# Optimization experiments

Hardware: AMD Instinct MI355X
Metric: run time of the kernel (lower is better)

## Reference

```python
import jax, jax.numpy as jnp
import numpy as np

B = 4096          # graphs (frames)
NPG = 22          # players per frame
N = B * NPG       # total nodes
E = B * NPG * (NPG - 1)
D_BB = 256        # backbone_dout == GRNN hidden
D_NODE = 128      # raw node feature dim
D_PROJ = 256      # cfg.proj_dout
D_GIN = 64        # glob_din
D_GOUT = 128      # cfg.glob_dout
D_IN = D_BB + D_PROJ  # GRNN input dim = 512


def setup_inputs() -> dict:
    key = jax.random.key(0)
    ks = jax.random.split(key, 24)
    def w(k, shape):
        return jax.random.normal(k, shape, jnp.float32) * 0.05
    inp = {
        "z": jax.random.normal(ks[0], (N, D_BB), jnp.float32),
        "u": jax.random.normal(ks[1], (B, D_GIN), jnp.float32),
        "x": jax.random.normal(ks[2], (N, D_NODE), jnp.float32),
        # edge_index is unused math-wise because GConvGRU is built with K=1 ChebConvs
        "edge_index": jax.random.randint(ks[3], (2, E), 0, N, dtype=jnp.int32),
        "batch": jnp.repeat(jnp.arange(B, dtype=jnp.int32), NPG),
        "batch_size": B,
        "prev_h": jax.random.normal(ks[4], (N, D_BB), jnp.float32),
        # fusion params
        "w_proj": w(ks[5], (D_NODE, D_PROJ)), "b_proj": jnp.zeros((D_PROJ,), jnp.float32),
        "w_glob": w(ks[6], (D_GIN, D_GOUT)), "b_glob": jnp.zeros((D_GOUT,), jnp.float32),
        # GConvGRU (K=1 ChebConv == linear) gate params: update z, reset r, candidate h
        "W_xz": w(ks[7], (D_IN, D_BB)),  "b_xz": jnp.zeros((D_BB,), jnp.float32),
        "W_hz": w(ks[8], (D_BB, D_BB)),  "b_hz": jnp.zeros((D_BB,), jnp.float32),
        "W_xr": w(ks[9], (D_IN, D_BB)),  "b_xr": jnp.zeros((D_BB,), jnp.float32),
        "W_hr": w(ks[10], (D_BB, D_BB)), "b_hr": jnp.zeros((D_BB,), jnp.float32),
        "W_xh": w(ks[11], (D_IN, D_BB)), "b_xh": jnp.zeros((D_BB,), jnp.float32),
        "W_hh": w(ks[12], (D_BB, D_BB)), "b_hh": jnp.zeros((D_BB,), jnp.float32),
    }
    return inp


def reference(z, u, x, edge_index, batch, batch_size, prev_h,
              w_proj, b_proj, w_glob, b_glob,
              W_xz, b_xz, W_hz, b_hz,
              W_xr, b_xr, W_hr, b_hr,
              W_xh, b_xh, W_hh, b_hh):
    # --- GraphGlobalFusion: mean readout + relu(Linear(u)) + concat ---
    sums = jax.ops.segment_sum(z, batch, num_segments=batch_size)            # [B, D_BB]
    cnts = jax.ops.segment_sum(jnp.ones((z.shape[0], 1), z.dtype), batch,
                               num_segments=batch_size)                      # [B, 1]
    graph_emb = sums / jnp.maximum(cnts, 1.0)
    glob_emb = jax.nn.relu(u @ w_glob + b_glob)                              # [B, D_GOUT]
    fused = jnp.concatenate([graph_emb, glob_emb], axis=-1)                  # [B, D_BB+D_GOUT]

    # --- node mode: raw feature projection, then GConvGRU (K=1 -> linear gates) ---
    x_proj = jax.nn.relu(x @ w_proj + b_proj)                                # [N, D_PROJ]
    xin = jnp.concatenate([z, x_proj], axis=-1)                              # [N, D_IN]
    Z = jax.nn.sigmoid(xin @ W_xz + b_xz + prev_h @ W_hz + b_hz)
    R = jax.nn.sigmoid(xin @ W_xr + b_xr + prev_h @ W_hr + b_hr)
    H_tilde = jnp.tanh(xin @ W_xh + b_xh + (prev_h * R) @ W_hh + b_hh)
    h = Z * prev_h + (1.0 - Z) * H_tilde                                     # [N, D_BB]
    return (fused, h)
```

## Files before the change

### kernel.cpp

```cpp
#include <hip/hip_runtime.h>
#include <hip/hip_bf16.h>

#define NNODES 90112
#define BGRAPH 4096
#define NPG 22
#define DBB 256
#define DNODE 128
#define DPROJ 256
#define DGIN 64
#define DGOUT 128

#define WTG_OFF   32768
#define WTHH_OFF  622592
#define WS_BF16_ELEMS 688128

typedef __attribute__((ext_vector_type(8))) short bf16x8;
typedef __attribute__((ext_vector_type(4))) short bf16x4;
typedef __attribute__((ext_vector_type(4))) float f32x4;
typedef __attribute__((ext_vector_type(2))) float f32x2;

__device__ __forceinline__ short f2bf(float f) {
  __hip_bfloat16 h = __float2bfloat16(f);
  return *reinterpret_cast<short*>(&h);
}
__device__ __forceinline__ float bf2f(short s) {
  union { unsigned int u; float f; } c;
  c.u = ((unsigned int)(unsigned short)s) << 16;
  return c.f;
}
__device__ __forceinline__ float fsig(float xv) {
  return __fdividef(1.0f, 1.0f + __expf(-xv));
}
__device__ __forceinline__ float ftanh(float xv) {
  return 1.0f - __fdividef(2.0f, __expf(2.0f * xv) + 1.0f);
}

#define DMA16(gsrc, ldst)                                                        \
  __builtin_amdgcn_global_load_lds(                                              \
      (const __attribute__((address_space(1))) void*)(gsrc),                     \
      (__attribute__((address_space(3))) void*)(ldst), 16, 0, 0)

template<int N>
__device__ __forceinline__ void vmwaitN() {
  static_assert(N >= 0 && N <= 6, "vmcnt range");
  if constexpr (N == 0) asm volatile("s_waitcnt vmcnt(0)" ::: "memory");
  else if constexpr (N == 1) asm volatile("s_waitcnt vmcnt(1)" ::: "memory");
  else if constexpr (N == 2) asm volatile("s_waitcnt vmcnt(2)" ::: "memory");
  else if constexpr (N == 3) asm volatile("s_waitcnt vmcnt(3)" ::: "memory");
  else if constexpr (N == 4) asm volatile("s_waitcnt vmcnt(4)" ::: "memory");
  else if constexpr (N == 5) asm volatile("s_waitcnt vmcnt(5)" ::: "memory");
  else asm volatile("s_waitcnt vmcnt(6)" ::: "memory");
  __builtin_amdgcn_sched_barrier(0);
}
#define LBAR() do { asm volatile("s_waitcnt lgkmcnt(0)" ::: "memory");           \
                    __builtin_amdgcn_s_barrier(); } while (0)

__global__ void pack_weights(const float* __restrict__ w_proj,
                             const float* __restrict__ W_xz, const float* __restrict__ W_hz,
                             const float* __restrict__ W_xr, const float* __restrict__ W_hr,
                             const float* __restrict__ W_xh, const float* __restrict__ W_hh,
                             const float* __restrict__ b_xz, const float* __restrict__ b_hz,
                             const float* __restrict__ b_xr, const float* __restrict__ b_hr,
                             const float* __restrict__ b_xh, const float* __restrict__ b_hh,
                             __hip_bfloat16* __restrict__ wsb, float* __restrict__ wsf) {
  int i = blockIdx.x * 256 + threadIdx.x;
  if (i < 32768) {
    int c = i >> 7, k = i & 127;
    wsb[i] = __float2bfloat16(w_proj[k * DPROJ + c]);
  } else if (i < WTHH_OFF) {
    int j = i - WTG_OFF;
    int kc  = j / 24576;
    int rem = j - kc * 24576;
    int ct  = rem >> 9;
    int q   = rem & 511;
    int l   = q >> 3, e = q & 7;
    int l15 = l & 15, kg = l >> 4;
    int k   = kc * 32 + kg * 8 + e;
    int g   = ct >> 4;
    int c   = (ct & 15) * 16 + l15;
    float v;
    if (g == 0)      v = (k < 512) ? W_xz[k * 256 + c] : W_hz[(k - 512) * 256 + c];
    else if (g == 1) v = (k < 512) ? W_xr[k * 256 + c] : W_hr[(k - 512) * 256 + c];
    else             v = (k < 512) ? W_xh[k * 256 + c] : 0.0f;
    wsb[i] = __float2bfloat16(v);
  } else if (i < WS_BF16_ELEMS) {
    int j = i - WTHH_OFF;
    int kc  = j >> 13;
    int rem = j & 8191;
    int ct  = rem >> 9;
    int q   = rem & 511;
    int l   = q >> 3, e = q & 7;
    int l15 = l & 15, kg = l >> 4;
    int k   = kc * 32 + kg * 8 + e;
    int c   = ct * 16 + l15;
    wsb[i] = __float2bfloat16(W_hh[k * 256 + c]);
  }
  if (i < 256) {
    wsf[i]       = b_xz[i] + b_hz[i];
    wsf[256 + i] = b_xr[i] + b_hr[i];
    wsf[512 + i] = b_xh[i] + b_hh[i];
  }
}

__global__ void fused_head(const float* __restrict__ z, const float* __restrict__ u,
                           const float* __restrict__ w_glob, const float* __restrict__ b_glob,
                           float* __restrict__ out) {
  int b = blockIdx.x;
  int t = threadIdx.x;
  __shared__ float us[DGIN];
  if (t < DGIN) us[t] = u[b * DGIN + t];
  __syncthreads();
  const float* zb = z + (size_t)b * NPG * DBB;
  #pragma unroll
  for (int half = 0; half < 2; ++half) {
    int c = t + half * 128;
    float s = 0.f;
    #pragma unroll
    for (int r = 0; r < NPG; ++r) s += zb[r * DBB + c];
    out[(size_t)b * 384 + c] = s * (1.0f / NPG);
  }
  float acc = b_glob[t];
  #pragma unroll
  for (int k = 0; k < DGIN; ++k) acc += us[k] * w_glob[k * DGOUT + t];
  out[(size_t)b * 384 + 256 + t] = fmaxf(acc, 0.f);
}

#define MFMA16(a, b, c) __builtin_amdgcn_mfma_f32_16x16x32_bf16(a, b, c, 0, 0, 0)

template<int KC>
__device__ __forceinline__ void gstep(
    const float* __restrict__ z, const float* __restrict__ prev_h,
    const __hip_bfloat16* __restrict__ wpk,
    __hip_bfloat16* Wb, __hip_bfloat16* ActC, __hip_bfloat16* XP,
    int tid, int r0, int l15, int lg, int wid, int lane,
    f32x4 (&accz)[4], f32x4 (&accr)[4], f32x4 (&acch)[4]) {
  constexpr int  KN       = KC + 1;
  constexpr bool do_stage = (KN >= 1 && KN <= 7) || (KN >= 16 && KN <= 23);
  constexpr bool bar      = (KC >= 1 && KC <= 7) || (KC >= 15 && KC <= 23);
  constexpr bool staged   = (KC < 8) || (KC >= 16);
  constexpr bool has_h    = (KC < 16);
  constexpr int NZ = (KC <= 14) ? 5 : (KC == 15) ? 4 : (KC <= 22) ? 3 : 1;
  constexpr int NR = (KC <= 14) ? 5 : (KC == 15) ? 4 : (KC <= 21) ? 3 : (KC == 22) ? 2 : 0;
  constexpr int NH = (KC <= 14) ? 5 : 4;

  f32x2 sl;
  int srow = tid >> 4, sc2 = (tid & 15) * 2;
  if constexpr (do_stage) {
    const float* src = (KN < 8) ? z : prev_h;
    constexpr int kofs = (KN < 8 ? KN : KN - 16) * 32;
    sl = *(const f32x2*)(src + (size_t)(r0 + srow) * DBB + kofs + sc2);
  }
  if constexpr (bar) LBAR();

  bf16x8 act[4];
  #pragma unroll
  for (int rt = 0; rt < 4; ++rt) {
    const int row = rt * 16 + l15;
    if constexpr (staged)
      act[rt] = *(const bf16x8*)&ActC[(KC % 3) * (64 * 40) + row * 40 + lg * 8];
    else {
      const int gk = (KC - 8) * 4 + lg;
      act[rt] = *(const bf16x8*)&XP[row * 256 + ((gk ^ (row & 7)) * 8)];
    }
  }

  vmwaitN<NZ>();
  {
    bf16x8 w = *(const bf16x8*)&Wb[((KC & 1) * 3 + 0) * 8192 + wid * 512 + lane * 8];
    __builtin_amdgcn_s_setprio(1);
    #pragma unroll
    for (int rt = 0; rt < 4; ++rt) accz[rt] = MFMA16(w, act[rt], accz[rt]);
    __builtin_amdgcn_s_setprio(0);
  }
  if constexpr (KC + 2 <= 23)
    DMA16(wpk + (((size_t)(KC + 2) * 48 + 0 * 16 + wid) * 64 + lane) * 8,
          Wb + (((KC + 2) & 1) * 3 + 0) * 8192 + wid * 512);

  vmwaitN<NR>();
  {
    bf16x8 w = *(const bf16x8*)&Wb[((KC & 1) * 3 + 1) * 8192 + wid * 512 + lane * 8];
    __builtin_amdgcn_s_setprio(1);
    #pragma unroll
    for (int rt = 0; rt < 4; ++rt) accr[rt] = MFMA16(w, act[rt], accr[rt]);
    __builtin_amdgcn_s_setprio(0);
  }
  if constexpr (KC + 2 <= 23)
    DMA16(wpk + (((size_t)(KC + 2) * 48 + 1 * 16 + wid) * 64 + lane) * 8,
          Wb + (((KC + 2) & 1) * 3 + 1) * 8192 + wid * 512);

  if constexpr (has_h) {
    vmwaitN<NH>();
    bf16x8 w = *(const bf16x8*)&Wb[((KC & 1) * 3 + 2) * 8192 + wid * 512 + lane * 8];
    __builtin_amdgcn_s_setprio(1);
    #pragma unroll
    for (int rt = 0; rt < 4; ++rt) acch[rt] = MFMA16(w, act[rt], acch[rt]);
    __builtin_amdgcn_s_setprio(0);
    if constexpr (KC + 2 <= 15)
      DMA16(wpk + (((size_t)(KC + 2) * 48 + 2 * 16 + wid) * 64 + lane) * 8,
            Wb + (((KC + 2) & 1) * 3 + 2) * 8192 + wid * 512);
  }

  if constexpr (do_stage) {
    unsigned int pk = (unsigned int)(unsigned short)f2bf(sl[0]) |
                      ((unsigned int)(unsigned short)f2bf(sl[1]) << 16);
    *(unsigned int*)&ActC[(KN % 3) * (64 * 40) + srow * 40 + sc2] = pk;
  }
}

template<int S>
__device__ __forceinline__ void hstep(
    const __hip_bfloat16* __restrict__ hpk, __hip_bfloat16* Wb, __hip_bfloat16* XP,
    int l15, int lg, int wid, int lane, f32x4 (&acch)[4]) {
  constexpr int NW = (S <= 5) ? 2 : (S == 6) ? 1 : 0;
  bf16x8 act[4];
  #pragma unroll
  for (int rt = 0; rt < 4; ++rt) {
    const int row = rt * 16 + l15;
    const int gk = S * 4 + lg;
    act[rt] = *(const bf16x8*)&XP[row * 256 + ((gk ^ (row & 7)) * 8)];
  }
  vmwaitN<NW>();
  bf16x8 w = *(const bf16x8*)&Wb[(S % 4) * 8192 + wid * 512 + lane * 8];
  __builtin_amdgcn_s_setprio(1);
  #pragma unroll
  for (int rt = 0; rt < 4; ++rt) acch[rt] = MFMA16(w, act[rt], acch[rt]);
  __builtin_amdgcn_s_setprio(0);
  if constexpr (S + 3 <= 7)
    DMA16(hpk + (((size_t)(S + 3) * 16 + wid) * 64 + lane) * 8,
          Wb + ((S + 3) % 4) * 8192 + wid * 512);
}

__global__ __launch_bounds__(1024)
void grnn_main(const float* __restrict__ z, const float* __restrict__ x,
               const float* __restrict__ prev_h, const float* __restrict__ b_proj,
               const __hip_bfloat16* __restrict__ wsb, const float* __restrict__ wsf,
               float* __restrict__ h_out) {
  __shared__ __align__(16) __hip_bfloat16 Wb[6 * 8192];
  __shared__ __align__(16) __hip_bfloat16 Xs[64 * 128];
  __shared__ __align__(16) __hip_bfloat16 XP[64 * 256];
  __shared__ __align__(16) __hip_bfloat16 ActC[3 * 64 * 40];

  const int r0   = blockIdx.x * 64;
  const int tid  = threadIdx.x;
  const int wid  = tid >> 6;
  const int lane = tid & 63;
  const int l15  = lane & 15;
  const int lg   = lane >> 4;
  const int c0   = wid * 16;
  const int cgrp = (c0 >> 3) + (lg >> 1);
  const int lgl  = (lg & 1) * 4;

  const __hip_bfloat16* wpk = wsb + WTG_OFF;
  const __hip_bfloat16* hpk = wsb + WTHH_OFF;

  {
    int row = tid >> 4, c8 = tid & 15;
    const float* p = x + (size_t)(r0 + row) * DNODE + c8 * 8;
    f32x4 f0 = *(const f32x4*)p;
    f32x4 f1 = *(const f32x4*)(p + 4);
    bf16x8 o;
    o[0]=f2bf(f0[0]); o[1]=f2bf(f0[1]); o[2]=f2bf(f0[2]); o[3]=f2bf(f0[3]);
    o[4]=f2bf(f1[0]); o[5]=f2bf(f1[1]); o[6]=f2bf(f1[2]); o[7]=f2bf(f1[3]);
    *(bf16x8*)&Xs[row * 128 + (c8 ^ (row & 7)) * 8] = o;
  }
  __syncthreads();

  f32x2 sl0;
  {
    int row = tid >> 4, c2 = (tid & 15) * 2;
    sl0 = *(const f32x2*)(z + (size_t)(r0 + row) * DBB + c2);
  }
  f32x4 accp[4] = {};
  {
    const __hip_bfloat16* wp0 = wsb + (size_t)(c0 + l15) * DNODE + lg * 8;
    #pragma unroll
    for (int kb = 0; kb < 4; ++kb) {
      bf16x8 wp = *(const bf16x8*)(wp0 + kb * 32);
      const int gk = kb * 4 + lg;
      bf16x8 act[4];
      #pragma unroll
      for (int rt = 0; rt < 4; ++rt) {
        const int row = rt * 16 + l15;
        act[rt] = *(const bf16x8*)&Xs[row * 128 + (gk ^ (row & 7)) * 8];
      }
      __builtin_amdgcn_s_setprio(1);
      #pragma unroll
      for (int rt = 0; rt < 4; ++rt)
        accp[rt] = MFMA16(wp, act[rt], accp[rt]);
      __builtin_amdgcn_s_setprio(0);
    }
  }
  #pragma unroll
  for (int c = 0; c < 2; ++c)
    #pragma unroll
    for (int g = 0; g < 3; ++g)
      DMA16(wpk + (((size_t)c * 48 + g * 16 + wid) * 64 + lane) * 8,
            Wb + ((c & 1) * 3 + g) * 8192 + wid * 512);
  {
    int row = tid >> 4, c2 = (tid & 15) * 2;
    unsigned int pk = (unsigned int)(unsigned short)f2bf(sl0[0]) |
                      ((unsigned int)(unsigned short)f2bf(sl0[1]) << 16);
    *(unsigned int*)&ActC[0 * (64 * 40) + row * 40 + c2] = pk;
  }
  {
    float4 bp4 = *(const float4*)&b_proj[c0 + lg * 4];
    #pragma unroll
    for (int rt = 0; rt < 4; ++rt) {
      int r = rt * 16 + l15;
      bf16x4 o;
      o[0] = f2bf(fmaxf(accp[rt][0] + bp4.x, 0.f));
      o[1] = f2bf(fmaxf(accp[rt][1] + bp4.y, 0.f));
      o[2] = f2bf(fmaxf(accp[rt][2] + bp4.z, 0.f));
      o[3] = f2bf(fmaxf(accp[rt][3] + bp4.w, 0.f));
      *(bf16x4*)&XP[r * 256 + ((cgrp ^ (r & 7)) * 8) + lgl] = o;
    }
  }
  LBAR();

  f32x4 accz[4] = {}, accr[4] = {}, acch[4] = {};
  #define GS(K) gstep<K>(z, prev_h, wpk, Wb, ActC, XP, tid, r0, l15, lg, wid, lane, accz, accr, acch)
  GS(0);  GS(1);  GS(2);  GS(3);  GS(4);  GS(5);  GS(6);  GS(7);
  GS(8);  GS(9);  GS(10); GS(11); GS(12); GS(13); GS(14); GS(15);
  GS(16); GS(17); GS(18); GS(19); GS(20); GS(21); GS(22); GS(23);
  #undef GS

  #pragma unroll
  for (int s = 0; s < 3; ++s)
    DMA16(hpk + (((size_t)s * 16 + wid) * 64 + lane) * 8, Wb + (s % 4) * 8192 + wid * 512);
  f32x4 phv[4];
  {
    float4 br4 = *(const float4*)&wsf[256 + c0 + lg * 4];
    #pragma unroll
    for (int rt = 0; rt < 4; ++rt) {
      int r = rt * 16 + l15;
      phv[rt] = *(const f32x4*)&prev_h[(size_t)(r0 + r) * DBB + c0 + lg * 4];
      bf16x4 o;
      o[0] = f2bf(phv[rt][0] * fsig(accr[rt][0] + br4.x));
      o[1] = f2bf(phv[rt][1] * fsig(accr[rt][1] + br4.y));
      o[2] = f2bf(phv[rt][2] * fsig(accr[rt][2] + br4.z));
      o[3] = f2bf(phv[rt][3] * fsig(accr[rt][3] + br4.w));
      *(bf16x4*)&XP[r * 256 + ((cgrp ^ (r & 7)) * 8) + lgl] = o;
    }
  }
  LBAR();

  #define HS(S) hstep<S>(hpk, Wb, XP, l15, lg, wid, lane, acch)
  HS(0); HS(1); HS(2); HS(3); HS(4); HS(5); HS(6); HS(7);
  #undef HS

  {
    float4 bz4 = *(const float4*)&wsf[c0 + lg * 4];
    float4 bh4 = *(const float4*)&wsf[512 + c0 + lg * 4];
    #pragma unroll
    for (int rt = 0; rt < 4; ++rt) {
      int r = rt * 16 + l15;
      f32x4 hv;
      float zg = fsig(accz[rt][0] + bz4.x);
      hv[0] = zg * phv[rt][0] + (1.f - zg) * ftanh(acch[rt][0] + bh4.x);
      zg = fsig(accz[rt][1] + bz4.y);
      hv[1] = zg * phv[rt][1] + (1.f - zg) * ftanh(acch[rt][1] + bh4.y);
      zg = fsig(accz[rt][2] + bz4.z);
      hv[2] = zg * phv[rt][2] + (1.f - zg) * ftanh(acch[rt][2] + bh4.z);
      zg = fsig(accz[rt][3] + bz4.w);
      hv[3] = zg * phv[rt][3] + (1.f - zg) * ftanh(acch[rt][3] + bh4.w);
      *(f32x4*)&h_out[(size_t)(r0 + r) * DBB + c0 + lg * 4] = hv;
    }
  }
}

extern "C" void kernel_launch(void* const* d_in, const int* in_sizes, int n_in,
                              void* d_out, int out_size, void* d_ws, size_t ws_size,
                              hipStream_t stream) {
  const float* z      = (const float*)d_in[0];
  const float* u      = (const float*)d_in[1];
  const float* x      = (const float*)d_in[2];
  const float* prev_h = (const float*)d_in[6];
  const float* w_proj = (const float*)d_in[7];
  const float* b_proj = (const float*)d_in[8];
  const float* w_glob = (const float*)d_in[9];
  const float* b_glob = (const float*)d_in[10];
  const float* W_xz   = (const float*)d_in[11];
  const float* b_xz   = (const float*)d_in[12];
  const float* W_hz   = (const float*)d_in[13];
  const float* b_hz   = (const float*)d_in[14];
  const float* W_xr   = (const float*)d_in[15];
  const float* b_xr   = (const float*)d_in[16];
  const float* W_hr   = (const float*)d_in[17];
  const float* b_hr   = (const float*)d_in[18];
  const float* W_xh   = (const float*)d_in[19];
  const float* b_xh   = (const float*)d_in[20];
  const float* W_hh   = (const float*)d_in[21];
  const float* b_hh   = (const float*)d_in[22];

  __hip_bfloat16* wsb = (__hip_bfloat16*)d_ws;
  float* wsf = (float*)((char*)d_ws + (size_t)WS_BF16_ELEMS * 2);

  float* fused = (float*)d_out;
  float* h_out = fused + (size_t)BGRAPH * 384;

  pack_weights<<<dim3(WS_BF16_ELEMS / 256), dim3(256), 0, stream>>>(
      w_proj, W_xz, W_hz, W_xr, W_hr, W_xh, W_hh,
      b_xz, b_hz, b_xr, b_hr, b_xh, b_hh, wsb, wsf);

  fused_head<<<dim3(BGRAPH), dim3(128), 0, stream>>>(z, u, w_glob, b_glob, fused);

  grnn_main<<<dim3(NNODES / 64), dim3(1024), 0, stream>>>(
      z, x, prev_h, b_proj, wsb, wsf, h_out);
}
```

Measured before the change: 211.4 us.

## Pair K-chunks per pipeline step with wider activation staging and fewer barriers

Restructures the fused GRU gate GEMM loop so each step processes two 32-wide K chunks, with fixed weight buffer slots per chunk parity. The z/r/h MFMAs are interleaved per row tile, and activation staging uses 4-float loads into a 6-slot ActC ring, so one stage covers two chunks. The separate Xs buffer is dropped by aliasing it onto ActC, which cuts shared memory. The goal is fewer LDS barriers and fewer wait points per K, plus more MFMA ILP, at the cost of a more complex vmcnt schedule that risks stalls or hazards if the counts are wrong.

```diff
diff --git a/kernel.cpp b/kernel.cpp
--- a/kernel.cpp
+++ b/kernel.cpp
@@ -17,7 +17,7 @@
 typedef __attribute__((ext_vector_type(8))) short bf16x8;
 typedef __attribute__((ext_vector_type(4))) short bf16x4;
 typedef __attribute__((ext_vector_type(4))) float f32x4;
-typedef __attribute__((ext_vector_type(2))) float f32x2;
+typedef __attribute__((ext_vector_type(2))) unsigned int u32x2;
 
 __device__ __forceinline__ short f2bf(float f) {
   __hip_bfloat16 h = __float2bfloat16(f);
@@ -127,83 +127,116 @@
 
 #define MFMA16(a, b, c) __builtin_amdgcn_mfma_f32_16x16x32_bf16(a, b, c, 0, 0, 0)
 
-template<int KC>
-__device__ __forceinline__ void gstep(
+__device__ __forceinline__ int spans_of(int c) { return c < 16 ? 3 : 2; }
+
+template<int J>
+__device__ __forceinline__ void jstep(
     const float* __restrict__ z, const float* __restrict__ prev_h,
     const __hip_bfloat16* __restrict__ wpk,
     __hip_bfloat16* Wb, __hip_bfloat16* ActC, __hip_bfloat16* XP,
     int tid, int r0, int l15, int lg, int wid, int lane,
     f32x4 (&accz)[4], f32x4 (&accr)[4], f32x4 (&acch)[4]) {
-  constexpr int  KN       = KC + 1;
-  constexpr bool do_stage = (KN >= 1 && KN <= 7) || (KN >= 16 && KN <= 23);
-  constexpr bool bar      = (KC >= 1 && KC <= 7) || (KC >= 15 && KC <= 23);
-  constexpr bool staged   = (KC < 8) || (KC >= 16);
-  constexpr bool has_h    = (KC < 16);
-  constexpr int NZ = (KC <= 14) ? 5 : (KC == 15) ? 4 : (KC <= 22) ? 3 : 1;
-  constexpr int NR = (KC <= 14) ? 5 : (KC == 15) ? 4 : (KC <= 21) ? 3 : (KC == 22) ? 2 : 0;
-  constexpr int NH = (KC <= 14) ? 5 : 4;
-
-  f32x2 sl;
-  int srow = tid >> 4, sc2 = (tid & 15) * 2;
-  if constexpr (do_stage) {
-    const float* src = (KN < 8) ? z : prev_h;
-    constexpr int kofs = (KN < 8 ? KN : KN - 16) * 32;
-    sl = *(const f32x2*)(src + (size_t)(r0 + srow) * DBB + kofs + sc2);
-  }
-  if constexpr (bar) LBAR();
-
-  bf16x8 act[4];
-  #pragma unroll
-  for (int rt = 0; rt < 4; ++rt) {
-    const int row = rt * 16 + l15;
-    if constexpr (staged)
-      act[rt] = *(const bf16x8*)&ActC[(KC % 3) * (64 * 40) + row * 40 + lg * 8];
-    else {
-      const int gk = (KC - 8) * 4 + lg;
-      act[rt] = *(const bf16x8*)&XP[row * 256 + ((gk ^ (row & 7)) * 8)];
-    }
-  }
-
-  vmwaitN<NZ>();
-  {
-    bf16x8 w = *(const bf16x8*)&Wb[((KC & 1) * 3 + 0) * 8192 + wid * 512 + lane * 8];
+  constexpr int  A   = 2 * J, B = 2 * J + 1;
+  constexpr bool S   = (J == 0) || (J == 1) || (J == 6) || (J == 7) || (J == 8) || (J == 9);
+  constexpr bool BAR = (J == 1) || (J == 2) || (J == 6) || (J == 7) || (J == 8) || (J == 9) || (J == 10);
+  constexpr int  sB  = (B < 16) ? 3 : 2;
+  constexpr int  c2  = (A + 2 <= 23) ? ((A + 2) < 16 ? 3 : 2) : 0;
+  constexpr int  d2  = (B + 2 <= 23) ? ((B + 2) < 16 ? 3 : 2) : 0;
+  constexpr bool hA  = (A < 16), hB = (B < 16);
+  constexpr bool actA = (A < 8) || (A >= 16);
+  constexpr bool actB = (B < 8) || (B >= 16);
+
+  f32x4 sl;
+  if constexpr (S) {
+    constexpr int C0 = 2 * J + 4;
+    const float* src = (C0 < 8) ? z : prev_h;
+    constexpr int kofs = (C0 < 8 ? C0 : C0 - 16) * 32;
+    const int srow = tid >> 4, skl = (tid & 15) * 4;
+    sl = *(const f32x4*)(src + (size_t)(r0 + srow) * DBB + kofs + skl);
+  }
+  if constexpr (BAR) LBAR();
+
+  {
+    bf16x8 act[4];
+    #pragma unroll
+    for (int rt = 0; rt < 4; ++rt) {
+      const int row = rt * 16 + l15;
+      if constexpr (actA)
+        act[rt] = *(const bf16x8*)&ActC[(A % 6) * 2560 + row * 40 + lg * 8];
+      else {
+        const int gk = (A - 8) * 4 + lg;
+        act[rt] = *(const bf16x8*)&XP[row * 256 + ((gk ^ (row & 7)) * 8)];
+      }
+    }
+    vmwaitN<sB + (S ? 1 : 0)>();
+    bf16x8 wz = *(const bf16x8*)&Wb[0 * 8192 + wid * 512 + lane * 8];
+    bf16x8 wr = *(const bf16x8*)&Wb[1 * 8192 + wid * 512 + lane * 8];
+    bf16x8 wh;
+    if constexpr (hA) wh = *(const bf16x8*)&Wb[2 * 8192 + wid * 512 + lane * 8];
     __builtin_amdgcn_s_setprio(1);
     #pragma unroll
-    for (int rt = 0; rt < 4; ++rt) accz[rt] = MFMA16(w, act[rt], accz[rt]);
+    for (int rt = 0; rt < 4; ++rt) {
+      accz[rt] = MFMA16(wz, act[rt], accz[rt]);
+      accr[rt] = MFMA16(wr, act[rt], accr[rt]);
+      if constexpr (hA) acch[rt] = MFMA16(wh, act[rt], acch[rt]);
+    }
     __builtin_amdgcn_s_setprio(0);
   }
-  if constexpr (KC + 2 <= 23)
-    DMA16(wpk + (((size_t)(KC + 2) * 48 + 0 * 16 + wid) * 64 + lane) * 8,
-          Wb + (((KC + 2) & 1) * 3 + 0) * 8192 + wid * 512);
-
-  vmwaitN<NR>();
-  {
-    bf16x8 w = *(const bf16x8*)&Wb[((KC & 1) * 3 + 1) * 8192 + wid * 512 + lane * 8];
+  if constexpr (A + 2 <= 23) {
+    #pragma unroll
+    for (int g = 0; g < 3; ++g)
+      if (g < ((A + 2) < 16 ? 3 : 2))
+        DMA16(wpk + (((size_t)(A + 2) * 48 + g * 16 + wid) * 64 + lane) * 8,
+              Wb + g * 8192 + wid * 512);
+  }
+
+  {
+    bf16x8 act[4];
+    #pragma unroll
+    for (int rt = 0; rt < 4; ++rt) {
+      const int row = rt * 16 + l15;
+      if constexpr (actB)
+        act[rt] = *(const bf16x8*)&ActC[(B % 6) * 2560 + row * 40 + lg * 8];
+      else {
+        const int gk = (B - 8) * 4 + lg;
+        act[rt] = *(const bf16x8*)&XP[row * 256 + ((gk ^ (row & 7)) * 8)];
+      }
+    }
+    vmwaitN<(S ? 1 : 0) + c2>();
+    bf16x8 wz = *(const bf16x8*)&Wb[3 * 8192 + wid * 512 + lane * 8];
+    bf16x8 wr = *(const bf16x8*)&Wb[4 * 8192 + wid * 512 + lane * 8];
+    bf16x8 wh;
+    if constexpr (hB) wh = *(const bf16x8*)&Wb[5 * 8192 + wid * 512 + lane * 8];
     __builtin_amdgcn_s_setprio(1);
     #pragma unroll
-    for (int rt = 0; rt < 4; ++rt) accr[rt] = MFMA16(w, act[rt], accr[rt]);
+    for (int rt = 0; rt < 4; ++rt) {
+      accz[rt] = MFMA16(wz, act[rt], accz[rt]);
+      accr[rt] = MFMA16(wr, act[rt], accr[rt]);
+      if constexpr (hB) acch[rt] = MFMA16(wh, act[rt], acch[rt]);
+    }
     __builtin_amdgcn_s_setprio(0);
   }
-  if constexpr (KC + 2 <= 23)
-    DMA16(wpk + (((size_t)(KC + 2) * 48 + 1 * 16 + wid) * 64 + lane) * 8,
-          Wb + (((KC + 2) & 1) * 3 + 1) * 8192 + wid * 512);
-
-  if constexpr (has_h) {
-    vmwaitN<NH>();
-    bf16x8 w = *(const bf16x8*)&Wb[((KC & 1) * 3 + 2) * 8192 + wid * 512 + lane * 8];
-    __builtin_amdgcn_s_setprio(1);
-    #pragma unroll
-    for (int rt = 0; rt < 4; ++rt) acch[rt] = MFMA16(w, act[rt], acch[rt]);
-    __builtin_amdgcn_s_setprio(0);
-    if constexpr (KC + 2 <= 15)
-      DMA16(wpk + (((size_t)(KC + 2) * 48 + 2 * 16 + wid) * 64 + lane) * 8,
-            Wb + (((KC + 2) & 1) * 3 + 2) * 8192 + wid * 512);
-  }
-
-  if constexpr (do_stage) {
-    unsigned int pk = (unsigned int)(unsigned short)f2bf(sl[0]) |
-                      ((unsigned int)(unsigned short)f2bf(sl[1]) << 16);
-    *(unsigned int*)&ActC[(KN % 3) * (64 * 40) + srow * 40 + sc2] = pk;
+  if constexpr (B + 2 <= 23) {
+    #pragma unroll
+    for (int g = 0; g < 3; ++g)
+      if (g < ((B + 2) < 16 ? 3 : 2))
+        DMA16(wpk + (((size_t)(B + 2) * 48 + g * 16 + wid) * 64 + lane) * 8,
+              Wb + (3 + g) * 8192 + wid * 512);
+  }
+
+  if constexpr (S) {
+    vmwaitN<c2 + d2>();
+    constexpr int C0 = 2 * J + 4;
+    constexpr int s0 = C0 % 6, s1 = (C0 + 1) % 6;
+    const int srow = tid >> 4, skl = (tid & 15) * 4;
+    const int s  = (skl < 32) ? s0 : s1;
+    const int kk = skl & 31;
+    u32x2 pk;
+    pk[0] = (unsigned int)(unsigned short)f2bf(sl[0]) |
+            ((unsigned int)(unsigned short)f2bf(sl[1]) << 16);
+    pk[1] = (unsigned int)(unsigned short)f2bf(sl[2]) |
+            ((unsigned int)(unsigned short)f2bf(sl[3]) << 16);
+    *(u32x2*)&ActC[s * 2560 + srow * 40 + kk] = pk;
   }
 }
 
@@ -236,9 +269,8 @@
                const __hip_bfloat16* __restrict__ wsb, const float* __restrict__ wsf,
                float* __restrict__ h_out) {
   __shared__ __align__(16) __hip_bfloat16 Wb[6 * 8192];
-  __shared__ __align__(16) __hip_bfloat16 Xs[64 * 128];
   __shared__ __align__(16) __hip_bfloat16 XP[64 * 256];
-  __shared__ __align__(16) __hip_bfloat16 ActC[3 * 64 * 40];
+  __shared__ __align__(16) __hip_bfloat16 ActC[6 * 2560];
 
   const int r0   = blockIdx.x * 64;
   const int tid  = threadIdx.x;
@@ -261,15 +293,10 @@
     bf16x8 o;
     o[0]=f2bf(f0[0]); o[1]=f2bf(f0[1]); o[2]=f2bf(f0[2]); o[3]=f2bf(f0[3]);
     o[4]=f2bf(f1[0]); o[5]=f2bf(f1[1]); o[6]=f2bf(f1[2]); o[7]=f2bf(f1[3]);
-    *(bf16x8*)&Xs[row * 128 + (c8 ^ (row & 7)) * 8] = o;
+    *(bf16x8*)&ActC[row * 128 + (c8 ^ (row & 7)) * 8] = o;
   }
   __syncthreads();
 
-  f32x2 sl0;
-  {
-    int row = tid >> 4, c2 = (tid & 15) * 2;
-    sl0 = *(const f32x2*)(z + (size_t)(r0 + row) * DBB + c2);
-  }
   f32x4 accp[4] = {};
   {
     const __hip_bfloat16* wp0 = wsb + (size_t)(c0 + l15) * DNODE + lg * 8;
@@ -281,7 +308,7 @@
       #pragma unroll
       for (int rt = 0; rt < 4; ++rt) {
         const int row = rt * 16 + l15;
-        act[rt] = *(const bf16x8*)&Xs[row * 128 + (gk ^ (row & 7)) * 8];
+        act[rt] = *(const bf16x8*)&ActC[row * 128 + (gk ^ (row & 7)) * 8];
       }
       __builtin_amdgcn_s_setprio(1);
       #pragma unroll
@@ -290,18 +317,20 @@
       __builtin_amdgcn_s_setprio(0);
     }
   }
-  #pragma unroll
-  for (int c = 0; c < 2; ++c)
-    #pragma unroll
-    for (int g = 0; g < 3; ++g)
-      DMA16(wpk + (((size_t)c * 48 + g * 16 + wid) * 64 + lane) * 8,
-            Wb + ((c & 1) * 3 + g) * 8192 + wid * 512);
-  {
-    int row = tid >> 4, c2 = (tid & 15) * 2;
-    unsigned int pk = (unsigned int)(unsigned short)f2bf(sl0[0]) |
-                      ((unsigned int)(unsigned short)f2bf(sl0[1]) << 16);
-    *(unsigned int*)&ActC[0 * (64 * 40) + row * 40 + c2] = pk;
-  }
+  f32x4 sl0, sl1;
+  {
+    int srow = tid >> 4, skl = (tid & 15) * 4;
+    sl0 = *(const f32x4*)(z + (size_t)(r0 + srow) * DBB + skl);
+    sl1 = *(const f32x4*)(z + (size_t)(r0 + srow) * DBB + 64 + skl);
+  }
+  #pragma unroll
+  for (int g = 0; g < 3; ++g)
+    DMA16(wpk + (((size_t)0 * 48 + g * 16 + wid) * 64 + lane) * 8,
+          Wb + g * 8192 + wid * 512);
+  #pragma unroll
+  for (int g = 0; g < 3; ++g)
+    DMA16(wpk + (((size_t)1 * 48 + g * 16 + wid) * 64 + lane) * 8,
+          Wb + (3 + g) * 8192 + wid * 512);
   {
     float4 bp4 = *(const float4*)&b_proj[c0 + lg * 4];
     #pragma unroll
@@ -316,13 +345,28 @@
     }
   }
   LBAR();
+  {
+    int srow = tid >> 4, skl = (tid & 15) * 4;
+    const int kk = skl & 31;
+    u32x2 pk;
+    pk[0] = (unsigned int)(unsigned short)f2bf(sl0[0]) |
+            ((unsigned int)(unsigned short)f2bf(sl0[1]) << 16);
+    pk[1] = (unsigned int)(unsigned short)f2bf(sl0[2]) |
+            ((unsigned int)(unsigned short)f2bf(sl0[3]) << 16);
+    *(u32x2*)&ActC[((skl < 32) ? 0 : 1) * 2560 + srow * 40 + kk] = pk;
+    pk[0] = (unsigned int)(unsigned short)f2bf(sl1[0]) |
+            ((unsigned int)(unsigned short)f2bf(sl1[1]) << 16);
+    pk[1] = (unsigned int)(unsigned short)f2bf(sl1[2]) |
+            ((unsigned int)(unsigned short)f2bf(sl1[3]) << 16);
+    *(u32x2*)&ActC[((skl < 32) ? 2 : 3) * 2560 + srow * 40 + kk] = pk;
+  }
+  LBAR();
 
   f32x4 accz[4] = {}, accr[4] = {}, acch[4] = {};
-  #define GS(K) gstep<K>(z, prev_h, wpk, Wb, ActC, XP, tid, r0, l15, lg, wid, lane, accz, accr, acch)
-  GS(0);  GS(1);  GS(2);  GS(3);  GS(4);  GS(5);  GS(6);  GS(7);
-  GS(8);  GS(9);  GS(10); GS(11); GS(12); GS(13); GS(14); GS(15);
-  GS(16); GS(17); GS(18); GS(19); GS(20); GS(21); GS(22); GS(23);
-  #undef GS
+  #define JS(K) jstep<K>(z, prev_h, wpk, Wb, ActC, XP, tid, r0, l15, lg, wid, lane, accz, accr, acch)
+  JS(0); JS(1); JS(2); JS(3); JS(4);  JS(5);
+  JS(6); JS(7); JS(8); JS(9); JS(10); JS(11);
+  #undef JS
 
   #pragma unroll
   for (int s = 0; s < 3; ++s)
```

Measured after the change: 225.7 us. 6.7% more time.
